# Performance work log

Hardware: AMD Instinct MI355X
Metric: run time of the kernel (lower is better)

Reference implementation:

```python
import math
import jax, jax.numpy as jnp
import numpy as np

NUM_HEADS = 32
NUM_KV_HEADS = 8
HEAD_DIM = 128
HIDDEN = 4096
ROPE_THETA = 500000.0
ROPE_FACTOR = 8.0
HIGH_FF = 4.0
LOW_FF = 1.0
ORIG_MAX_POS = 8192


def _llama3_inv_freq():
    # Llama-3 rope frequency scaling
    inv = 1.0 / (ROPE_THETA ** (np.arange(0, HEAD_DIM, 2, dtype=np.float32) / HEAD_DIM))
    wavelen = 2.0 * np.pi / inv
    low_wl = ORIG_MAX_POS / LOW_FF
    high_wl = ORIG_MAX_POS / HIGH_FF
    inv_scaled = np.where(wavelen > low_wl, inv / ROPE_FACTOR, inv)
    smooth = (ORIG_MAX_POS / wavelen - LOW_FF) / (HIGH_FF - LOW_FF)
    smoothed = (1.0 - smooth) / ROPE_FACTOR * inv + smooth * inv
    is_medium = (wavelen <= low_wl) & (wavelen >= high_wl)
    return jnp.asarray(np.where(is_medium, smoothed, inv_scaled), dtype=jnp.float32)


def _rotate_half(x):
    h = x.shape[-1] // 2
    return jnp.concatenate([-x[..., h:], x[..., :h]], axis=-1)


def setup_inputs() -> dict:
    key = jax.random.key(0)
    ks = jax.random.split(key, 5)
    s = 0.02
    return {
        "x": jax.random.normal(ks[0], (1, 2048, HIDDEN), dtype=jnp.float32),
        "Wq": jax.random.normal(ks[1], (NUM_HEADS * HEAD_DIM, HIDDEN), dtype=jnp.float32) * s,
        "Wk": jax.random.normal(ks[2], (NUM_KV_HEADS * HEAD_DIM, HIDDEN), dtype=jnp.float32) * s,
        "Wv": jax.random.normal(ks[3], (NUM_KV_HEADS * HEAD_DIM, HIDDEN), dtype=jnp.float32) * s,
        "Wo": jax.random.normal(ks[4], (HIDDEN, NUM_HEADS * HEAD_DIM), dtype=jnp.float32) * s,
    }


def reference(x, Wq, Wk, Wv, Wo):
    B, T, _ = x.shape
    G = NUM_HEADS // NUM_KV_HEADS  # query heads per kv head

    q = jnp.einsum("bth,oh->bto", x, Wq).reshape(B, T, NUM_HEADS, HEAD_DIM).transpose(0, 2, 1, 3)
    k = jnp.einsum("bth,oh->bto", x, Wk).reshape(B, T, NUM_KV_HEADS, HEAD_DIM).transpose(0, 2, 1, 3)
    v = jnp.einsum("bth,oh->bto", x, Wv).reshape(B, T, NUM_KV_HEADS, HEAD_DIM).transpose(0, 2, 1, 3)

    # RoPE (past_len = 0, prefill)
    inv_freq = _llama3_inv_freq()
    pos = jnp.arange(T, dtype=jnp.float32)
    freqs = pos[:, None] * inv_freq[None, :]             # [T, D/2]
    emb = jnp.concatenate([freqs, freqs], axis=-1)       # [T, D]
    cos, sin = jnp.cos(emb), jnp.sin(emb)
    q = q * cos + _rotate_half(q) * sin
    k = k * cos + _rotate_half(k) * sin

    # GQA attention: group query heads over kv heads instead of repeat_interleave
    qg = q.reshape(B, NUM_KV_HEADS, G, T, HEAD_DIM)
    scale = 1.0 / math.sqrt(HEAD_DIM)
    scores = jnp.einsum("bkgtd,bksd->bkgts", qg, k) * scale  # [B,Hkv,G,T,T]
    causal = jnp.tril(jnp.ones((T, T), dtype=bool))
    scores = jnp.where(causal, scores, -jnp.inf)
    attn = jax.nn.softmax(scores, axis=-1)
    out = jnp.einsum("bkgts,bksd->bkgtd", attn, v)           # [B,Hkv,G,T,D]
    out = out.reshape(B, NUM_HEADS, T, HEAD_DIM).transpose(0, 2, 1, 3).reshape(B, T, NUM_HEADS * HEAD_DIM)
    return jnp.einsum("bto,ho->bth", out, Wo)
```

## Files before the change

### kernel.cpp

```cpp
#include <hip/hip_runtime.h>
#include <math.h>

#define T 2048
#define HID 4096
#define NH 32
#define NKV 8
#define HD 128
#define QSCALE 0.08838834764831845f

typedef __attribute__((ext_vector_type(8))) short short8;
typedef __attribute__((ext_vector_type(4))) float f32x4;
typedef __attribute__((ext_vector_type(16))) float f32x16;

static __device__ __forceinline__ unsigned short f2bf(float f) {
  union { float f; unsigned u; } v; v.f = f;
  unsigned r = v.u;
  r += 0x7fffu + ((r >> 16) & 1u);
  return (unsigned short)(r >> 16);
}

static __device__ __forceinline__ void async_cp16(const unsigned short* g, unsigned short* l) {
  __builtin_amdgcn_global_load_lds(
      (const __attribute__((address_space(1))) void*)g,
      (__attribute__((address_space(3))) void*)l,
      16, 0, 0);
}

__global__ __launch_bounds__(256) void cast4_kernel(const float* __restrict__ s0, const float* __restrict__ s1,
                                                    const float* __restrict__ s2, const float* __restrict__ s3,
                                                    unsigned short* __restrict__ d0, unsigned short* __restrict__ d1,
                                                    unsigned short* __restrict__ d2, unsigned short* __restrict__ d3,
                                                    int n0, int n1, int n2, int n3) {
  int i = blockIdx.x * 256 + threadIdx.x;
  const float* s; unsigned short* d; int j = i;
  if (j < n0) { s = s0; d = d0; }
  else { j -= n0;
    if (j < n1) { s = s1; d = d1; }
    else { j -= n1;
      if (j < n2) { s = s2; d = d2; }
      else { j -= n2;
        if (j >= n3) return;
        s = s3; d = d3; } } }
  float4 f = ((const float4*)s)[j];
  ushort4 o;
  o.x = f2bf(f.x); o.y = f2bf(f.y); o.z = f2bf(f.z); o.w = f2bf(f.w);
  ((ushort4*)d)[j] = o;
}


static __device__ __forceinline__ short8 ldfrag(const unsigned short* tile, int row0, int ks, int lane) {
  int row = row0 + (lane & 15);
  int slot = (ks * 4 + (lane >> 4)) ^ (lane & 7);
  return *(const short8*)&tile[row * 64 + slot * 8];
}

static __device__ __forceinline__ void ldb2(short8 (&b)[2][2], const unsigned short* bs, int br0, int lane) {
#pragma unroll
  for (int j = 0; j < 2; j++)
#pragma unroll
    for (int ks = 0; ks < 2; ks++)
      b[j][ks] = ldfrag(bs, br0 + j * 16, ks, lane);
}

template <int H>
static __device__ __forceinline__ void preA(short8 (&a)[4][2], const unsigned short* as, int ar, int lane) {
#pragma unroll
  for (int m = 2 * H; m < 2 * H + 2; m++)
#pragma unroll
    for (int ks = 0; ks < 2; ks++)
      a[m][ks] = ldfrag(as, ar + m * 16, ks, lane);
}

template <int P, int NF>
static __device__ __forceinline__ void mfma16(const short8 (&a)[4][2], const short8 (&b)[2][2],
                                              f32x4 (&acc)[4][2 * NF]) {
  __builtin_amdgcn_s_setprio(1);
#pragma unroll
  for (int ks = 0; ks < 2; ks++)
#pragma unroll
    for (int m = 0; m < 4; m++)
#pragma unroll
      for (int j = 0; j < 2; j++)
        acc[m][P * 2 + j] = __builtin_amdgcn_mfma_f32_16x16x32_bf16(
            a[m][ks], b[j][ks], acc[m][P * 2 + j], 0, 0, 0);
  __builtin_amdgcn_s_setprio(0);
}

#define SCHED0 __builtin_amdgcn_sched_barrier(0)
#define BAR_PRE  do { SCHED0; __builtin_amdgcn_s_barrier(); \
                      asm volatile("s_waitcnt lgkmcnt(0)" ::: "memory"); SCHED0; } while (0)
#define BAR_POST do { SCHED0; __builtin_amdgcn_s_barrier(); SCHED0; } while (0)
#define VMCNT(n) asm volatile("s_waitcnt vmcnt(" #n ")" ::: "memory")

template <int NF>
static __device__ __forceinline__ void tile_body(
    short8 (&aC)[4][2], short8 (&aN)[4][2],
    const unsigned short* bsRd, unsigned short* bsSt,
    const unsigned short* asN, unsigned short* asS,
    const unsigned short* const (&baseA)[4], const unsigned short* const (&baseB)[NF],
    int kA, int kB, int ar, int br, int wave, int lane,
    f32x4 (&acc)[4][2 * NF]) {
  short8 b[2][2];
  if constexpr (NF == 3) {
    ldb2(b, bsRd, br + 0, lane);
    async_cp16(baseB[0] + kB, bsSt + 0 * 4096 + wave * 512);
    async_cp16(baseB[1] + kB, bsSt + 1 * 4096 + wave * 512);
    async_cp16(baseB[2] + kB, bsSt + 2 * 4096 + wave * 512);
    BAR_PRE; mfma16<0, NF>(aC, b, acc); BAR_POST;
    ldb2(b, bsRd, br + 32, lane);
    preA<0>(aN, asN, ar, lane);
    async_cp16(baseA[0] + kA, asS + 0 * 4096 + wave * 512);
    async_cp16(baseA[1] + kA, asS + 1 * 4096 + wave * 512);
    BAR_PRE; mfma16<1, NF>(aC, b, acc); BAR_POST;
    ldb2(b, bsRd, br + 64, lane);
    preA<1>(aN, asN, ar, lane);
    async_cp16(baseA[2] + kA, asS + 2 * 4096 + wave * 512);
    async_cp16(baseA[3] + kA, asS + 3 * 4096 + wave * 512);
    VMCNT(4);
    BAR_PRE; mfma16<2, NF>(aC, b, acc); BAR_POST;
  } else {
    ldb2(b, bsRd, br + 0, lane);
    preA<0>(aN, asN, ar, lane);
    async_cp16(baseB[0] + kB, bsSt + 0 * 4096 + wave * 512);
    async_cp16(baseB[1] + kB, bsSt + 1 * 4096 + wave * 512);
    BAR_PRE; mfma16<0, NF>(aC, b, acc); BAR_POST;
    ldb2(b, bsRd, br + 32, lane);
    preA<1>(aN, asN, ar, lane);
    async_cp16(baseA[0] + kA, asS + 0 * 4096 + wave * 512);
    async_cp16(baseA[1] + kA, asS + 1 * 4096 + wave * 512);
    async_cp16(baseA[2] + kA, asS + 2 * 4096 + wave * 512);
    async_cp16(baseA[3] + kA, asS + 3 * 4096 + wave * 512);
    VMCNT(6);
    BAR_PRE; mfma16<1, NF>(aC, b, acc); BAR_POST;
  }
}

template <int NF>
__global__ __launch_bounds__(512, 2) void gemm9(const unsigned short* __restrict__ A,
                                                const unsigned short* __restrict__ Bt,
                                                float* __restrict__ C,
                                                int M, int N, int K) {
  __shared__ __align__(16) unsigned short AsBuf[3][16384];
  __shared__ __align__(16) unsigned short BsBuf[NF == 3 ? 2 : 3][NF * 4096];
  int tid = threadIdx.x, wave = tid >> 6, lane = tid & 63;
  int wm = wave >> 1, wn = wave & 1;
  long bm0 = (long)blockIdx.y * 256, bn0 = (long)blockIdx.x * (NF * 64);
  int ar = wm * 64, br = wn * (NF * 32);

  long stRow = wave * 8 + (lane >> 3);
  int slot = ((lane & 7) ^ (lane >> 3)) * 8;
  const unsigned short* baseA[4];
#pragma unroll
  for (int c = 0; c < 4; c++) baseA[c] = A + (bm0 + c * 64 + stRow) * (long)K + slot;
  const unsigned short* baseB[NF];
#pragma unroll
  for (int c = 0; c < NF; c++) baseB[c] = Bt + (bn0 + c * 64 + stRow) * (long)K + slot;

  int nkt = K >> 6;
  f32x4 acc[4][2 * NF] = {};
  short8 aX[4][2], aY[4][2];
  unsigned short *as0 = AsBuf[0], *as1 = AsBuf[1], *as2 = AsBuf[2];

  if constexpr (NF == 3) {
#pragma unroll
    for (int c = 0; c < 3; c++) async_cp16(baseB[c], &BsBuf[0][c * 4096 + wave * 512]);
#pragma unroll
    for (int c = 0; c < 4; c++) async_cp16(baseA[c], as0 + c * 4096 + wave * 512);
#pragma unroll
    for (int c = 0; c < 4; c++) async_cp16(baseA[c] + 64, as1 + c * 4096 + wave * 512);
#pragma unroll
    for (int c = 0; c < 4; c++) async_cp16(baseA[c] + 128, as2 + c * 4096 + wave * 512);
    VMCNT(4);
    SCHED0; __builtin_amdgcn_s_barrier(); SCHED0;
    preA<0>(aX, as0, ar, lane); preA<1>(aX, as0, ar, lane);
#pragma unroll 1
    for (int it = 0; it < (nkt >> 1); ++it) {
      int t = 2 * it;
      int kA0 = ((t + 3) < nkt ? (t + 3) : (nkt - 1)) << 6;
      int kB0 = ((t + 1) < nkt ? (t + 1) : (nkt - 1)) << 6;
      tile_body<3>(aX, aY, BsBuf[0], BsBuf[1], as1, as0, baseA, baseB, kA0, kB0, ar, br, wave, lane, acc);
      int kA1 = ((t + 4) < nkt ? (t + 4) : (nkt - 1)) << 6;
      int kB1 = ((t + 2) < nkt ? (t + 2) : (nkt - 1)) << 6;
      tile_body<3>(aY, aX, BsBuf[1], BsBuf[0], as2, as1, baseA, baseB, kA1, kB1, ar, br, wave, lane, acc);
      unsigned short* tA = as0; as0 = as2; as2 = as1; as1 = tA;
    }
  } else {
    unsigned short *bs0 = BsBuf[0], *bs1 = BsBuf[1], *bs2 = BsBuf[2];
#pragma unroll
    for (int c = 0; c < 2; c++) async_cp16(baseB[c], bs0 + c * 4096 + wave * 512);
#pragma unroll
    for (int c = 0; c < 4; c++) async_cp16(baseA[c], as0 + c * 4096 + wave * 512);
#pragma unroll
    for (int c = 0; c < 2; c++) async_cp16(baseB[c] + 64, bs1 + c * 4096 + wave * 512);
#pragma unroll
    for (int c = 0; c < 4; c++) async_cp16(baseA[c] + 64, as1 + c * 4096 + wave * 512);
#pragma unroll
    for (int c = 0; c < 4; c++) async_cp16(baseA[c] + 128, as2 + c * 4096 + wave * 512);
    VMCNT(4);
    SCHED0; __builtin_amdgcn_s_barrier(); SCHED0;
    preA<0>(aX, as0, ar, lane); preA<1>(aX, as0, ar, lane);
#pragma unroll 1
    for (int it = 0; it < (nkt >> 1); ++it) {
      int t = 2 * it;
      int kA0 = ((t + 3) < nkt ? (t + 3) : (nkt - 1)) << 6;
      int kB0 = ((t + 2) < nkt ? (t + 2) : (nkt - 1)) << 6;
      tile_body<2>(aX, aY, bs0, bs2, as1, as0, baseA, baseB, kA0, kB0, ar, br, wave, lane, acc);
      int kA1 = ((t + 4) < nkt ? (t + 4) : (nkt - 1)) << 6;
      int kB1 = ((t + 3) < nkt ? (t + 3) : (nkt - 1)) << 6;
      tile_body<2>(aY, aX, bs1, bs0, as2, as1, baseA, baseB, kA1, kB1, ar, br, wave, lane, acc);
      unsigned short* tA = as0; as0 = as2; as2 = as1; as1 = tA;
      unsigned short* tB = bs0; bs0 = bs2; bs2 = bs1; bs1 = tB;
    }
  }
  VMCNT(0);

#pragma unroll
  for (int m = 0; m < 4; m++)
#pragma unroll
    for (int n = 0; n < 2 * NF; n++) {
      long row = bm0 + ar + m * 16 + ((lane >> 4) << 2);
      long col = bn0 + br + n * 16 + (lane & 15);
#pragma unroll
      for (int j = 0; j < 4; j++)
        C[(row + j) * (long)N + col] = acc[m][n][j];
    }
}

__global__ __launch_bounds__(256) void aux_kernel(const float* __restrict__ qkvf,
                                                  unsigned short* __restrict__ qb,
                                                  unsigned short* __restrict__ kb,
                                                  unsigned short* __restrict__ vtb,
                                                  const float* __restrict__ Wo,
                                                  unsigned short* __restrict__ wo_bf) {
  __shared__ float tile[64][33];
  int b = blockIdx.x;
  if (b < 20480) {
    int bx = b & 511, hh = b >> 9;
    int lt = threadIdx.x >> 6, d = threadIdx.x & 63;
    int t = bx * 4 + lt;
    float ex = (float)d * (1.0f / 64.0f);
    float inv = expf(-ex * 13.122363377404328f);
    float wl = 6.283185307179586f / inv;
    float inv_s;
    if (wl > 8192.0f)       inv_s = inv * 0.125f;
    else if (wl < 2048.0f)  inv_s = inv;
    else {
      float smooth = (8192.0f / wl - 1.0f) * (1.0f / 3.0f);
      inv_s = (1.0f - smooth) * 0.125f * inv + smooth * inv;
    }
    float ang = (float)t * inv_s;
    float s, c;
    sincosf(ang, &s, &c);
    if (hh < NH) {
      const float* base = qkvf + (long)t * 6144 + hh * HD;
      float lo = base[d], hi = base[d + 64];
      long o = ((long)hh * T + t) * HD;
      qb[o + d]      = f2bf((lo * c - hi * s) * QSCALE);
      qb[o + d + 64] = f2bf((hi * c + lo * s) * QSCALE);
    } else {
      int h = hh - NH;
      const float* base = qkvf + (long)t * 6144 + 4096 + h * HD;
      float lo = base[d], hi = base[d + 64];
      long o = ((long)h * T + t) * HD;
      kb[o + d]      = f2bf(lo * c - hi * s);
      kb[o + d + 64] = f2bf(hi * c + lo * s);
    }
  } else if (b < 21504) {
    int b2 = b - 20480;
    int t0 = (b2 & 31) * 64, d0 = ((b2 >> 5) & 3) * 32, h = b2 >> 7;
    int tid = threadIdx.x;
    int dd = tid & 31, tt = tid >> 5;
#pragma unroll
    for (int i = 0; i < 8; i++) {
      int t = tt + i * 8;
      tile[t][dd] = qkvf[(long)(t0 + t) * 6144 + 5120 + h * HD + d0 + dd];
    }
    __syncthreads();
    int t2 = tid & 63, d2 = tid >> 6;
#pragma unroll
    for (int i = 0; i < 8; i++) {
      int d = d2 + i * 4;
      vtb[((long)(h * HD + d0 + d)) * T + t0 + t2] = f2bf(tile[t2][d]);
    }
  } else {
    int j = (b - 21504) * 256 + threadIdx.x;
    float4 f = ((const float4*)Wo)[j];
    ushort4 o;
    o.x = f2bf(f.x); o.y = f2bf(f.y); o.z = f2bf(f.z); o.w = f2bf(f.w);
    ((ushort4*)wo_bf)[j] = o;
  }
}

__global__ __launch_bounds__(256, 2) void attn_kernel(const unsigned short* __restrict__ qb,
                                                      const unsigned short* __restrict__ kbuf,
                                                      const unsigned short* __restrict__ vtb,
                                                      unsigned short* __restrict__ ob) {
  __shared__ __align__(16) unsigned short Ks[2][64 * 128];
  __shared__ __align__(16) unsigned short Vs[2][128 * 64];
  __shared__ __align__(16) unsigned short Ps[4][32 * 64];
  int h = blockIdx.y;
  int kvh = h >> 2;
  int qt = (blockIdx.y >= 16) ? (int)(gridDim.x - 1 - blockIdx.x) : (int)blockIdx.x;
  int q0 = qt * 128;
  int tid = threadIdx.x, wave = tid >> 6, lane = tid & 63;
  int l31 = lane & 31, half = lane >> 5;
  const unsigned short* Kb = kbuf + (long)kvh * T * HD;
  const unsigned short* Vb = vtb + (long)kvh * HD * T;

  auto STAGE = [&](int tile, int bf) {
    int kb0 = tile * 64;
#pragma unroll
    for (int i = 0; i < 4; i++) {
      int c = wave * 4 + i;
      { int row = c * 4 + (lane >> 4);
        int g = (lane & 15) ^ (row & 15);
        async_cp16(&Kb[(long)(kb0 + row) * HD + g * 8], &Ks[bf][c * 512]); }
      { int row = c * 8 + (lane >> 3);
        int g = (lane & 7) ^ (row & 7);
        async_cp16(&Vb[(long)row * T + kb0 + g * 8], &Vs[bf][c * 512]); }
    }
  };

  STAGE(0, 0);

  int qrow = q0 + wave * 32 + l31;
  short8 aq[8];
#pragma unroll
  for (int ks = 0; ks < 8; ks++)
    aq[ks] = *(const short8*)&qb[((long)h * T + qrow) * HD + ks * 16 + half * 8];

  f32x16 oacc[4] = {};
  float psum[16];
#pragma unroll
  for (int r = 0; r < 16; r++) psum[r] = 0.0f;

  int ntiles = 2 * qt + 2;
  for (int tile = 0; tile < ntiles; tile++) {
    int cur = tile & 1;
    if (tile + 1 < ntiles) {
      STAGE(tile + 1, cur ^ 1);
      asm volatile("s_waitcnt vmcnt(8)" ::: "memory");
    } else {
      asm volatile("s_waitcnt vmcnt(0)" ::: "memory");
    }
    SCHED0; __builtin_amdgcn_s_barrier(); SCHED0;

    f32x16 sacc[2] = {};
#pragma unroll
    for (int ks = 0; ks < 8; ks++)
#pragma unroll
      for (int nt = 0; nt < 2; nt++) {
        int row = nt * 32 + l31;
        short8 bk = *(const short8*)&Ks[cur][row * 128 + (((2 * ks + half) ^ (row & 15)) * 8)];
        sacc[nt] = __builtin_amdgcn_mfma_f32_32x32x16_bf16(aq[ks], bk, sacc[nt], 0, 0, 0);
      }

    int kb0 = tile * 64;
    if (kb0 + 63 > q0 + wave * 32) {
#pragma unroll
      for (int nt = 0; nt < 2; nt++) {
        int key = kb0 + nt * 32 + l31;
#pragma unroll
        for (int r = 0; r < 16; r++) {
          int qr = q0 + wave * 32 + (r & 3) + 8 * (r >> 2) + 4 * half;
          if (key > qr) sacc[nt][r] = -3.0e38f;
        }
      }
    }

#pragma unroll
    for (int nt = 0; nt < 2; nt++)
#pragma unroll
      for (int r = 0; r < 16; r++) {
        float p = __expf(sacc[nt][r]);
        psum[r] += p;
        int prow = (r & 3) + 8 * (r >> 2) + 4 * half;
        Ps[wave][prow * 64 + ((nt * 32 + l31) ^ ((prow & 7) << 3))] = f2bf(p);
      }

#pragma unroll
    for (int ks = 0; ks < 4; ks++) {
      short8 ap = *(const short8*)&Ps[wave][l31 * 64 + (((ks * 2 + half) ^ (l31 & 7)) * 8)];
#pragma unroll
      for (int nt = 0; nt < 4; nt++) {
        int row = nt * 32 + l31;
        short8 bv = *(const short8*)&Vs[cur][row * 64 + (((2 * ks + half) ^ (row & 7)) * 8)];
        oacc[nt] = __builtin_amdgcn_mfma_f32_32x32x16_bf16(ap, bv, oacc[nt], 0, 0, 0);
      }
    }
    SCHED0; __builtin_amdgcn_s_barrier(); SCHED0;
  }

#pragma unroll
  for (int off = 1; off <= 16; off <<= 1)
#pragma unroll
    for (int r = 0; r < 16; r++)
      psum[r] += __shfl_xor(psum[r], off, 64);

#pragma unroll
  for (int nt = 0; nt < 4; nt++)
#pragma unroll
    for (int r = 0; r < 16; r++) {
      int row = q0 + wave * 32 + (r & 3) + 8 * (r >> 2) + 4 * half;
      ob[(long)row * HID + h * HD + nt * 32 + l31] = f2bf(oacc[nt][r] / psum[r]);
    }
}

extern "C" void kernel_launch(void* const* d_in, const int* in_sizes, int n_in,
                              void* d_out, int out_size, void* d_ws, size_t ws_size,
                              hipStream_t stream) {
  const float* x  = (const float*)d_in[0];
  const float* Wq = (const float*)d_in[1];
  const float* Wk = (const float*)d_in[2];
  const float* Wv = (const float*)d_in[3];
  const float* Wo = (const float*)d_in[4];
  float* out = (float*)d_out;

  char* ws = (char*)d_ws;
  size_t off = 0;
  auto alloc = [&](size_t bytes) {
    char* p = ws + off;
    off += (bytes + 255) & ~(size_t)255;
    return p;
  };
  unsigned short* x_bf    = (unsigned short*)alloc((size_t)T * HID * 2);
  unsigned short* wqkv_bf = (unsigned short*)alloc((size_t)6144 * HID * 2);
  float* qkvf = (float*)alloc((size_t)T * 6144 * 4);
  unsigned short* qb  = (unsigned short*)alloc((size_t)NH * T * HD * 2);
  unsigned short* kbb = (unsigned short*)alloc((size_t)NKV * T * HD * 2);
  unsigned short* vtb = (unsigned short*)alloc((size_t)NKV * HD * T * 2);
  unsigned short* obb = (unsigned short*)alloc((size_t)T * HID * 2);

  int n0 = T * HID / 4, n1 = HID * HID / 4, n2 = 1024 * HID / 4, n3 = 1024 * HID / 4;
  int ntot = n0 + n1 + n2 + n3;
  cast4_kernel<<<dim3((ntot + 255) / 256), dim3(256), 0, stream>>>(
      x, Wq, Wk, Wv,
      x_bf, wqkv_bf, wqkv_bf + (size_t)HID * HID, wqkv_bf + (size_t)5120 * HID,
      n0, n1, n2, n3);

  gemm9<3><<<dim3(6144 / 192, T / 256), dim3(512), 0, stream>>>(x_bf, wqkv_bf, qkvf, T, 6144, HID);

  aux_kernel<<<dim3(37888), dim3(256), 0, stream>>>(qkvf, qb, kbb, vtb, Wo, wqkv_bf);

  attn_kernel<<<dim3(T / 128, NH), dim3(256), 0, stream>>>(qb, kbb, vtb, obb);
  gemm9<2><<<dim3(HID / 128, T / 256), dim3(512), 0, stream>>>(obb, wqkv_bf, out, T, HID, HID);
}
```

Before: 447.0 us.

## Replace triple-buffered interleaved GEMM pipeline with simple double-buffered loop

Swaps the hand-scheduled GEMM, which used triple-buffered A tiles, register-prefetched A fragments and several barriers with MFMA bursts per k-tile, for a plain double-buffered loop. Each k-tile now issues async loads for the next tile, waits on vmcnt and a barrier, loads all fragments, then runs all MFMAs. Launch bounds drop from 2 to 1 blocks per CU, and the s_setprio hints are removed. The aim is less barrier and scheduling overhead, at the cost of shallower prefetch and less overlap between LDS reads and MFMA.

Result: slower. 474.4 us (+6.1%).

```diff
diff --git a/kernel.cpp b/kernel.cpp
--- a/kernel.cpp
+++ b/kernel.cpp
@@ -25,6 +25,9 @@
       (__attribute__((address_space(3))) void*)l,
       16, 0, 0);
 }
+
+#define SCHED0 __builtin_amdgcn_sched_barrier(0)
+#define VMCNT(n) asm volatile("s_waitcnt vmcnt(" #n ")" ::: "memory")
 
 __global__ __launch_bounds__(256) void cast4_kernel(const float* __restrict__ s0, const float* __restrict__ s1,
                                                     const float* __restrict__ s2, const float* __restrict__ s3,
@@ -54,94 +57,14 @@
   return *(const short8*)&tile[row * 64 + slot * 8];
 }
 
-static __device__ __forceinline__ void ldb2(short8 (&b)[2][2], const unsigned short* bs, int br0, int lane) {
-#pragma unroll
-  for (int j = 0; j < 2; j++)
-#pragma unroll
-    for (int ks = 0; ks < 2; ks++)
-      b[j][ks] = ldfrag(bs, br0 + j * 16, ks, lane);
-}
-
-template <int H>
-static __device__ __forceinline__ void preA(short8 (&a)[4][2], const unsigned short* as, int ar, int lane) {
-#pragma unroll
-  for (int m = 2 * H; m < 2 * H + 2; m++)
-#pragma unroll
-    for (int ks = 0; ks < 2; ks++)
-      a[m][ks] = ldfrag(as, ar + m * 16, ks, lane);
-}
-
-template <int P, int NF>
-static __device__ __forceinline__ void mfma16(const short8 (&a)[4][2], const short8 (&b)[2][2],
-                                              f32x4 (&acc)[4][2 * NF]) {
-  __builtin_amdgcn_s_setprio(1);
-#pragma unroll
-  for (int ks = 0; ks < 2; ks++)
-#pragma unroll
-    for (int m = 0; m < 4; m++)
-#pragma unroll
-      for (int j = 0; j < 2; j++)
-        acc[m][P * 2 + j] = __builtin_amdgcn_mfma_f32_16x16x32_bf16(
-            a[m][ks], b[j][ks], acc[m][P * 2 + j], 0, 0, 0);
-  __builtin_amdgcn_s_setprio(0);
-}
-
-#define SCHED0 __builtin_amdgcn_sched_barrier(0)
-#define BAR_PRE  do { SCHED0; __builtin_amdgcn_s_barrier(); \
-                      asm volatile("s_waitcnt lgkmcnt(0)" ::: "memory"); SCHED0; } while (0)
-#define BAR_POST do { SCHED0; __builtin_amdgcn_s_barrier(); SCHED0; } while (0)
-#define VMCNT(n) asm volatile("s_waitcnt vmcnt(" #n ")" ::: "memory")
-
 template <int NF>
-static __device__ __forceinline__ void tile_body(
-    short8 (&aC)[4][2], short8 (&aN)[4][2],
-    const unsigned short* bsRd, unsigned short* bsSt,
-    const unsigned short* asN, unsigned short* asS,
-    const unsigned short* const (&baseA)[4], const unsigned short* const (&baseB)[NF],
-    int kA, int kB, int ar, int br, int wave, int lane,
-    f32x4 (&acc)[4][2 * NF]) {
-  short8 b[2][2];
-  if constexpr (NF == 3) {
-    ldb2(b, bsRd, br + 0, lane);
-    async_cp16(baseB[0] + kB, bsSt + 0 * 4096 + wave * 512);
-    async_cp16(baseB[1] + kB, bsSt + 1 * 4096 + wave * 512);
-    async_cp16(baseB[2] + kB, bsSt + 2 * 4096 + wave * 512);
-    BAR_PRE; mfma16<0, NF>(aC, b, acc); BAR_POST;
-    ldb2(b, bsRd, br + 32, lane);
-    preA<0>(aN, asN, ar, lane);
-    async_cp16(baseA[0] + kA, asS + 0 * 4096 + wave * 512);
-    async_cp16(baseA[1] + kA, asS + 1 * 4096 + wave * 512);
-    BAR_PRE; mfma16<1, NF>(aC, b, acc); BAR_POST;
-    ldb2(b, bsRd, br + 64, lane);
-    preA<1>(aN, asN, ar, lane);
-    async_cp16(baseA[2] + kA, asS + 2 * 4096 + wave * 512);
-    async_cp16(baseA[3] + kA, asS + 3 * 4096 + wave * 512);
-    VMCNT(4);
-    BAR_PRE; mfma16<2, NF>(aC, b, acc); BAR_POST;
-  } else {
-    ldb2(b, bsRd, br + 0, lane);
-    preA<0>(aN, asN, ar, lane);
-    async_cp16(baseB[0] + kB, bsSt + 0 * 4096 + wave * 512);
-    async_cp16(baseB[1] + kB, bsSt + 1 * 4096 + wave * 512);
-    BAR_PRE; mfma16<0, NF>(aC, b, acc); BAR_POST;
-    ldb2(b, bsRd, br + 32, lane);
-    preA<1>(aN, asN, ar, lane);
-    async_cp16(baseA[0] + kA, asS + 0 * 4096 + wave * 512);
-    async_cp16(baseA[1] + kA, asS + 1 * 4096 + wave * 512);
-    async_cp16(baseA[2] + kA, asS + 2 * 4096 + wave * 512);
-    async_cp16(baseA[3] + kA, asS + 3 * 4096 + wave * 512);
-    VMCNT(6);
-    BAR_PRE; mfma16<1, NF>(aC, b, acc); BAR_POST;
-  }
-}
-
-template <int NF>
-__global__ __launch_bounds__(512, 2) void gemm9(const unsigned short* __restrict__ A,
-                                                const unsigned short* __restrict__ Bt,
-                                                float* __restrict__ C,
-                                                int M, int N, int K) {
-  __shared__ __align__(16) unsigned short AsBuf[3][16384];
-  __shared__ __align__(16) unsigned short BsBuf[NF == 3 ? 2 : 3][NF * 4096];
+__global__ __launch_bounds__(512, 1) void gemm11(const unsigned short* __restrict__ A,
+                                                 const unsigned short* __restrict__ Bt,
+                                                 float* __restrict__ C,
+                                                 int M, int N, int K) {
+  constexpr int NB = 2 * NF;
+  __shared__ __align__(16) unsigned short As[2][16384];
+  __shared__ __align__(16) unsigned short Bs[2][NF * 4096];
   int tid = threadIdx.x, wave = tid >> 6, lane = tid & 63;
   int wm = wave >> 1, wn = wave & 1;
   long bm0 = (long)blockIdx.y * 256, bn0 = (long)blockIdx.x * (NF * 64);
@@ -157,67 +80,50 @@
   for (int c = 0; c < NF; c++) baseB[c] = Bt + (bn0 + c * 64 + stRow) * (long)K + slot;
 
   int nkt = K >> 6;
-  f32x4 acc[4][2 * NF] = {};
-  short8 aX[4][2], aY[4][2];
-  unsigned short *as0 = AsBuf[0], *as1 = AsBuf[1], *as2 = AsBuf[2];
-
-  if constexpr (NF == 3) {
-#pragma unroll
-    for (int c = 0; c < 3; c++) async_cp16(baseB[c], &BsBuf[0][c * 4096 + wave * 512]);
-#pragma unroll
-    for (int c = 0; c < 4; c++) async_cp16(baseA[c], as0 + c * 4096 + wave * 512);
-#pragma unroll
-    for (int c = 0; c < 4; c++) async_cp16(baseA[c] + 64, as1 + c * 4096 + wave * 512);
-#pragma unroll
-    for (int c = 0; c < 4; c++) async_cp16(baseA[c] + 128, as2 + c * 4096 + wave * 512);
-    VMCNT(4);
+  f32x4 acc[4][NB] = {};
+
+#pragma unroll
+  for (int c = 0; c < 4; c++) async_cp16(baseA[c], &As[0][c * 4096 + wave * 512]);
+#pragma unroll
+  for (int c = 0; c < NF; c++) async_cp16(baseB[c], &Bs[0][c * 4096 + wave * 512]);
+
+#pragma unroll 1
+  for (int t = 0; t < nkt; ++t) {
+    int tn = (t + 1 < nkt) ? (t + 1) : (nkt - 1);
+    int kn = tn << 6;
+#pragma unroll
+    for (int c = 0; c < 4; c++) async_cp16(baseA[c] + kn, &As[(t + 1) & 1][c * 4096 + wave * 512]);
+#pragma unroll
+    for (int c = 0; c < NF; c++) async_cp16(baseB[c] + kn, &Bs[(t + 1) & 1][c * 4096 + wave * 512]);
+    if constexpr (NF == 3) { VMCNT(7); } else { VMCNT(6); }
     SCHED0; __builtin_amdgcn_s_barrier(); SCHED0;
-    preA<0>(aX, as0, ar, lane); preA<1>(aX, as0, ar, lane);
-#pragma unroll 1
-    for (int it = 0; it < (nkt >> 1); ++it) {
-      int t = 2 * it;
-      int kA0 = ((t + 3) < nkt ? (t + 3) : (nkt - 1)) << 6;
-      int kB0 = ((t + 1) < nkt ? (t + 1) : (nkt - 1)) << 6;
-      tile_body<3>(aX, aY, BsBuf[0], BsBuf[1], as1, as0, baseA, baseB, kA0, kB0, ar, br, wave, lane, acc);
-      int kA1 = ((t + 4) < nkt ? (t + 4) : (nkt - 1)) << 6;
-      int kB1 = ((t + 2) < nkt ? (t + 2) : (nkt - 1)) << 6;
-      tile_body<3>(aY, aX, BsBuf[1], BsBuf[0], as2, as1, baseA, baseB, kA1, kB1, ar, br, wave, lane, acc);
-      unsigned short* tA = as0; as0 = as2; as2 = as1; as1 = tA;
-    }
-  } else {
-    unsigned short *bs0 = BsBuf[0], *bs1 = BsBuf[1], *bs2 = BsBuf[2];
-#pragma unroll
-    for (int c = 0; c < 2; c++) async_cp16(baseB[c], bs0 + c * 4096 + wave * 512);
-#pragma unroll
-    for (int c = 0; c < 4; c++) async_cp16(baseA[c], as0 + c * 4096 + wave * 512);
-#pragma unroll
-    for (int c = 0; c < 2; c++) async_cp16(baseB[c] + 64, bs1 + c * 4096 + wave * 512);
-#pragma unroll
-    for (int c = 0; c < 4; c++) async_cp16(baseA[c] + 64, as1 + c * 4096 + wave * 512);
-#pragma unroll
-    for (int c = 0; c < 4; c++) async_cp16(baseA[c] + 128, as2 + c * 4096 + wave * 512);
-    VMCNT(4);
+
+    const unsigned short* as = As[t & 1];
+    const unsigned short* bs = Bs[t & 1];
+    short8 a[4][2], b[NB][2];
+#pragma unroll
+    for (int m = 0; m < 4; m++)
+#pragma unroll
+      for (int ks = 0; ks < 2; ks++) a[m][ks] = ldfrag(as, ar + m * 16, ks, lane);
+#pragma unroll
+    for (int n = 0; n < NB; n++)
+#pragma unroll
+      for (int ks = 0; ks < 2; ks++) b[n][ks] = ldfrag(bs, br + n * 16, ks, lane);
+#pragma unroll
+    for (int ks = 0; ks < 2; ks++)
+#pragma unroll
+      for (int m = 0; m < 4; m++)
+#pragma unroll
+        for (int n = 0; n < NB; n++)
+          acc[m][n] = __builtin_amdgcn_mfma_f32_16x16x32_bf16(a[m][ks], b[n][ks], acc[m][n], 0, 0, 0);
     SCHED0; __builtin_amdgcn_s_barrier(); SCHED0;
-    preA<0>(aX, as0, ar, lane); preA<1>(aX, as0, ar, lane);
-#pragma unroll 1
-    for (int it = 0; it < (nkt >> 1); ++it) {
-      int t = 2 * it;
-      int kA0 = ((t + 3) < nkt ? (t + 3) : (nkt - 1)) << 6;
-      int kB0 = ((t + 2) < nkt ? (t + 2) : (nkt - 1)) << 6;
-      tile_body<2>(aX, aY, bs0, bs2, as1, as0, baseA, baseB, kA0, kB0, ar, br, wave, lane, acc);
-      int kA1 = ((t + 4) < nkt ? (t + 4) : (nkt - 1)) << 6;
-      int kB1 = ((t + 3) < nkt ? (t + 3) : (nkt - 1)) << 6;
-      tile_body<2>(aY, aX, bs1, bs0, as2, as1, baseA, baseB, kA1, kB1, ar, br, wave, lane, acc);
-      unsigned short* tA = as0; as0 = as2; as2 = as1; as1 = tA;
-      unsigned short* tB = bs0; bs0 = bs2; bs2 = bs1; bs1 = tB;
-    }
   }
   VMCNT(0);
 
 #pragma unroll
   for (int m = 0; m < 4; m++)
 #pragma unroll
-    for (int n = 0; n < 2 * NF; n++) {
+    for (int n = 0; n < NB; n++) {
       long row = bm0 + ar + m * 16 + ((lane >> 4) << 2);
       long col = bn0 + br + n * 16 + (lane & 15);
 #pragma unroll
@@ -438,10 +344,10 @@
       x_bf, wqkv_bf, wqkv_bf + (size_t)HID * HID, wqkv_bf + (size_t)5120 * HID,
       n0, n1, n2, n3);
 
-  gemm9<3><<<dim3(6144 / 192, T / 256), dim3(512), 0, stream>>>(x_bf, wqkv_bf, qkvf, T, 6144, HID);
+  gemm11<3><<<dim3(6144 / 192, T / 256), dim3(512), 0, stream>>>(x_bf, wqkv_bf, qkvf, T, 6144, HID);
 
   aux_kernel<<<dim3(37888), dim3(256), 0, stream>>>(qkvf, qb, kbb, vtb, Wo, wqkv_bf);
 
   attn_kernel<<<dim3(T / 128, NH), dim3(256), 0, stream>>>(qb, kbb, vtb, obb);
-  gemm9<2><<<dim3(HID / 128, T / 256), dim3(512), 0, stream>>>(obb, wqkv_bf, out, T, HID, HID);
-}
+  gemm11<2><<<dim3(HID / 128, T / 256), dim3(512), 0, stream>>>(obb, wqkv_bf, out, T, HID, HID);
+}
```
